# Performance work log

Hardware: AMD Instinct MI355X
Metric: run time of the kernel (lower is better)

## Reference

```python
import jax, jax.numpy as jnp
import numpy as np

B, S, HID = 4, 2048, 2048
H, HKV, D = 16, 4, 128
RANK = 512
SCALE = D ** -0.5


def setup_inputs() -> dict:
    key = jax.random.key(0)
    ks = jax.random.split(key, 5)
    scale_w = 0.02
    return {
        "hidden_states": jax.random.normal(ks[0], (B, S, HID), dtype=jnp.float32),
        "Wq": jax.random.normal(ks[1], (HID, H * D), dtype=jnp.float32) * scale_w,
        "Wc": jax.random.normal(ks[2], (HID, RANK), dtype=jnp.float32) * scale_w,
        "Wup": jax.random.normal(ks[3], (RANK, HKV * D), dtype=jnp.float32) * scale_w,
        "Wo": jax.random.normal(ks[4], (H * D, HID), dtype=jnp.float32) * scale_w,
    }


def reference(hidden_states, Wq, Wc, Wup, Wo):
    b, s, _ = hidden_states.shape
    n_rep = H // HKV
    # Q projection -> (b, H, s, D)
    q = (hidden_states @ Wq).reshape(b, s, H, D).transpose(0, 2, 1, 3)
    # low-rank KV compression -> (b, s, RANK)
    kv_c = hidden_states @ Wc
    # gate in source is ones -> sigmoid(1) constant scalar multiply
    kv_c = kv_c * jax.nn.sigmoid(jnp.float32(1.0))
    # decompress: single kv_up_proj produces shared K/V content
    kv = (kv_c @ Wup).reshape(b, s, HKV, D).transpose(0, 2, 1, 3)  # (b, HKV, s, D)
    k = jnp.repeat(kv, n_rep, axis=1)  # (b, H, s, D), repeat_interleave over heads
    v = k
    scores = jnp.einsum("bhqd,bhkd->bhqk", q, k) * SCALE
    attn = jax.nn.softmax(scores.astype(jnp.float32), axis=-1).astype(q.dtype)
    out = jnp.einsum("bhqk,bhkd->bhqd", attn, v)
    out = out.transpose(0, 2, 1, 3).reshape(b, s, H * D)
    return out @ Wo
```

## Files before the change

kernel.cpp:

```cpp
#include <hip/hip_runtime.h>
#include <hip/hip_bf16.h>
#include <stdint.h>

#define DEV __device__ __forceinline__

typedef __bf16 bf16x8 __attribute__((ext_vector_type(8)));
typedef float f32x4 __attribute__((ext_vector_type(4)));
typedef float f32x16 __attribute__((ext_vector_type(16)));
typedef int i32x4 __attribute__((ext_vector_type(4)));


DEV void gload_lds16(const void* g, void* l) {
  __builtin_amdgcn_global_load_lds((const __attribute__((address_space(1))) void*)g,
                                   (__attribute__((address_space(3))) void*)l, 16, 0, 0);
}

__global__ __launch_bounds__(256) void k_cast(const float* __restrict__ in,
                                              __hip_bfloat16* __restrict__ out, int n) {
  int i = (blockIdx.x * 256 + threadIdx.x) * 8;
  if (i >= n) return;
  const float4* p = (const float4*)(in + i);
  float4 a = p[0], c = p[1];
  bf16x8 v;
  v[0] = (__bf16)a.x; v[1] = (__bf16)a.y; v[2] = (__bf16)a.z; v[3] = (__bf16)a.w;
  v[4] = (__bf16)c.x; v[5] = (__bf16)c.y; v[6] = (__bf16)c.z; v[7] = (__bf16)c.w;
  *(bf16x8*)(out + i) = v;
}

__global__ __launch_bounds__(256) void k_tcast(const float* __restrict__ in,
                                               __hip_bfloat16* __restrict__ out, int R, int C) {
  __shared__ float t[32][33];
  int c0 = blockIdx.x * 32, r0 = blockIdx.y * 32;
  int x = threadIdx.x, y0 = threadIdx.y;
  for (int j = y0; j < 32; j += 8) t[j][x] = in[(size_t)(r0 + j) * C + c0 + x];
  __syncthreads();
  for (int j = y0; j < 32; j += 8)
    out[(size_t)(c0 + j) * R + r0 + x] = __float2bfloat16(t[x][j]);
}

__global__ __launch_bounds__(256) void k_tbf16(const __hip_bfloat16* __restrict__ in,
                                               __hip_bfloat16* __restrict__ out) {
  __shared__ unsigned short t[32][33];
  int z = blockIdx.z;
  const unsigned short* ip = (const unsigned short*)in + (size_t)z * 2048 * 128;
  unsigned short* op = (unsigned short*)out + (size_t)z * 2048 * 128;
  int d0 = blockIdx.x * 32, s0 = blockIdx.y * 32;
  int x = threadIdx.x, y0 = threadIdx.y;
  for (int j = y0; j < 32; j += 8) t[j][x] = ip[(size_t)(s0 + j) * 128 + d0 + x];
  __syncthreads();
  for (int j = y0; j < 32; j += 8) op[(size_t)(d0 + j) * 2048 + s0 + x] = t[x][j];
}

template <int MODE>
__global__ __launch_bounds__(256, 2) void k_gemm(const __hip_bfloat16* __restrict__ A,
                                                 const __hip_bfloat16* __restrict__ BT,
                                                 void* __restrict__ Cout,
                                                 int M, int N, int K, float scale) {
  __shared__ __align__(16) __hip_bfloat16 As[128 * 64];
  __shared__ __align__(16) __hip_bfloat16 Bs[128 * 64];
  const int tid = threadIdx.x;
  const int lane = tid & 63, wid = tid >> 6;
  const int g = lane >> 4, lr = lane & 15;
  const int m0 = blockIdx.x * 128, n0 = blockIdx.y * 128;
  const int wr = wid >> 1, wc = wid & 1;
  const f32x4 vzero = {0.f, 0.f, 0.f, 0.f};

  f32x4 acc[4][4];
#pragma unroll
  for (int i = 0; i < 4; ++i)
#pragma unroll
    for (int j = 0; j < 4; ++j) acc[i][j] = vzero;

  const char* aSrc[4];
  const char* bSrc[4];
  char* aDst[4];
  char* bDst[4];
#pragma unroll
  for (int i = 0; i < 4; ++i) {
    int p = i * 4096 + tid * 16;
    int row = p >> 7, colb = p & 127;
    int scol = colb ^ ((row & 7) << 4);
    aSrc[i] = (const char*)A + ((size_t)(m0 + row) * K) * 2 + scol;
    bSrc[i] = (const char*)BT + ((size_t)(n0 + row) * K) * 2 + scol;
    aDst[i] = (char*)As + i * 4096 + wid * 1024;
    bDst[i] = (char*)Bs + i * 4096 + wid * 1024;
  }

  const int nk = K >> 6;
  for (int kt = 0; kt < nk; ++kt) {
    const size_t ko = (size_t)kt * 128;
#pragma unroll
    for (int i = 0; i < 4; ++i) gload_lds16(aSrc[i] + ko, aDst[i]);
#pragma unroll
    for (int i = 0; i < 4; ++i) gload_lds16(bSrc[i] + ko, bDst[i]);
    __syncthreads();
#pragma unroll
    for (int kc = 0; kc < 2; ++kc) {
      bf16x8 af[4], bfr[4];
#pragma unroll
      for (int fm = 0; fm < 4; ++fm) {
        int row = wr * 64 + fm * 16 + lr;
        int cb = (kc * 64 + g * 16) ^ ((row & 7) << 4);
        af[fm] = *(const bf16x8*)((const char*)As + row * 128 + cb);
      }
#pragma unroll
      for (int fn = 0; fn < 4; ++fn) {
        int row = wc * 64 + fn * 16 + lr;
        int cb = (kc * 64 + g * 16) ^ ((row & 7) << 4);
        bfr[fn] = *(const bf16x8*)((const char*)Bs + row * 128 + cb);
      }
#pragma unroll
      for (int fm = 0; fm < 4; ++fm)
#pragma unroll
        for (int fn = 0; fn < 4; ++fn)
          acc[fm][fn] =
              __builtin_amdgcn_mfma_f32_16x16x32_bf16(af[fm], bfr[fn], acc[fm][fn], 0, 0, 0);
    }
    __syncthreads();
  }

#pragma unroll
  for (int fm = 0; fm < 4; ++fm) {
#pragma unroll
    for (int fn = 0; fn < 4; ++fn) {
      const int mb = m0 + wr * 64 + fm * 16 + g * 4;
      const int n = n0 + wc * 64 + fn * 16 + lr;
#pragma unroll
      for (int r = 0; r < 4; ++r) {
        float v = acc[fm][fn][r] * scale;
        int m = mb + r;
        if constexpr (MODE == 0) {
          ((float*)Cout)[(size_t)m * N + n] = v;
        } else if constexpr (MODE == 1) {
          int b = m >> 11, s = m & 2047, h = n >> 7, d = n & 127;
          ((__hip_bfloat16*)Cout)[(((size_t)(b * 16 + h) * 2048) + s) * 128 + d] =
              __float2bfloat16(v);
        } else if constexpr (MODE == 2) {
          int b = m >> 11, s = m & 2047, hk = n >> 7, d = n & 127;
          ((__hip_bfloat16*)Cout)[(((size_t)(b * 4 + hk) * 2048) + s) * 128 + d] =
              __float2bfloat16(v);
        } else {
          ((__hip_bfloat16*)Cout)[(size_t)n * M + m] = __float2bfloat16(v);
        }
      }
    }
  }
}

__global__ __launch_bounds__(512, 2) void k_attn2(const __hip_bfloat16* __restrict__ q,
                                                  const __hip_bfloat16* __restrict__ kv,
                                                  const __hip_bfloat16* __restrict__ kvT,
                                                  __hip_bfloat16* __restrict__ out) {
  __shared__ __align__(16) char smem[65536];
  const int tid = threadIdx.x, lane = tid & 63, wid = tid >> 6;
  const int hi = lane >> 5, lq = lane & 31;
  const int qt = blockIdx.x;
  const int pair = blockIdx.y;
  const int b = pair >> 2, hkv = pair & 3;
  const int h = hkv * 4 + (wid & 3);
  const int q0w = qt * 64 + (wid >> 2) * 32;

  const char* qrow =
      (const char*)q + (((size_t)(b * 16 + h) * 2048 + q0w + lq) * 128 + hi * 8) * 2;
  bf16x8 qfr[8];
#pragma unroll
  for (int kt = 0; kt < 8; ++kt) qfr[kt] = *(const bf16x8*)(qrow + kt * 32);

  const char* kbase = (const char*)kv + ((size_t)pair * 2048 * 128) * 2;
  const char* tbase = (const char*)kvT + ((size_t)pair * 2048 * 128) * 2;
  const char* pK;
  const char* pV;
  {
    int p0 = tid * 16;
    int krow = p0 >> 8, kcol = p0 & 255;
    pK = kbase + (size_t)krow * 256 + (kcol ^ ((krow & 15) << 4));
    int vrow = p0 >> 7, vcol = p0 & 127;
    pV = tbase + (size_t)vrow * 4096 + (vcol ^ ((vrow & 7) << 4));
  }

  f32x16 accO[4];
#pragma unroll
  for (int dt = 0; dt < 4; ++dt)
#pragma unroll
    for (int i = 0; i < 16; ++i) accO[dt][i] = 0.f;
  float m_run = -1e30f, l_run = 0.f;

  const int hsK = (hi * 16) ^ ((lq & 15) << 4);
  const int hsV = (hi * 16) ^ ((lq & 7) << 4);

  auto stage = [&](int kb, int vb) {
    gload_lds16(pK, smem + kb + wid * 1024);
    gload_lds16(pK + 8192, smem + kb + 8192 + wid * 1024);
    gload_lds16(pV, smem + vb + wid * 1024);
    gload_lds16(pV + 262144, smem + vb + 8192 + wid * 1024);
    pK += 16384;
    pV += 128;
  };

  auto compute = [&](int kb, int vb) {
    f32x16 st[2];
#pragma unroll
    for (int i = 0; i < 16; ++i) { st[0][i] = 0.f; st[1][i] = 0.f; }
    const char* Kb = smem + kb;
#pragma unroll
    for (int tau = 0; tau < 2; ++tau) {
      const char* Kr = Kb + (tau * 32 + lq) * 256;
#pragma unroll
      for (int kt = 0; kt < 8; ++kt) {
        bf16x8 kf = *(const bf16x8*)(Kr + ((kt * 32) ^ hsK));
        st[tau] = __builtin_amdgcn_mfma_f32_32x32x16_bf16(kf, qfr[kt], st[tau], 0, 0, 0);
      }
    }
    float mloc[8];
#pragma unroll
    for (int i = 0; i < 8; ++i)
      mloc[i] = fmaxf(fmaxf(st[0][i], st[0][i + 8]), fmaxf(st[1][i], st[1][i + 8]));
#pragma unroll
    for (int i = 0; i < 4; ++i) mloc[i] = fmaxf(mloc[i], mloc[i + 4]);
    float pm = fmaxf(fmaxf(mloc[0], mloc[1]), fmaxf(mloc[2], mloc[3]));
    pm = fmaxf(pm, __shfl_xor(pm, 32));
    if (__any(pm > m_run + 8.f)) {
      float mnew = fmaxf(m_run, pm);
      float alpha = __builtin_amdgcn_exp2f(m_run - mnew);
      m_run = mnew;
      l_run *= alpha;
#pragma unroll
      for (int dt = 0; dt < 4; ++dt)
#pragma unroll
        for (int i = 0; i < 16; ++i) accO[dt][i] *= alpha;
    }
    float p0[16], p1[16];
#pragma unroll
    for (int i = 0; i < 16; ++i) p0[i] = __builtin_amdgcn_exp2f(st[0][i] - m_run);
#pragma unroll
    for (int i = 0; i < 16; ++i) p1[i] = __builtin_amdgcn_exp2f(st[1][i] - m_run);
    float s0 = 0.f, s1 = 0.f, s2 = 0.f, s3 = 0.f;
#pragma unroll
    for (int i = 0; i < 8; ++i) {
      s0 += p0[i]; s1 += p0[i + 8]; s2 += p1[i]; s3 += p1[i + 8];
    }
    l_run += (s0 + s1) + (s2 + s3);
    bf16x8 pfr[4];
#pragma unroll
    for (int ks = 0; ks < 4; ++ks) {
      const int base = (ks & 1) * 8;
      int A0, A1, B0, B1;
      if (ks < 2) {
        asm("v_cvt_pk_bf16_f32 %0, %1, %2" : "=v"(A0) : "v"(p0[base + 0]), "v"(p0[base + 1]));
        asm("v_cvt_pk_bf16_f32 %0, %1, %2" : "=v"(A1) : "v"(p0[base + 2]), "v"(p0[base + 3]));
        asm("v_cvt_pk_bf16_f32 %0, %1, %2" : "=v"(B0) : "v"(p0[base + 4]), "v"(p0[base + 5]));
        asm("v_cvt_pk_bf16_f32 %0, %1, %2" : "=v"(B1) : "v"(p0[base + 6]), "v"(p0[base + 7]));
      } else {
        asm("v_cvt_pk_bf16_f32 %0, %1, %2" : "=v"(A0) : "v"(p1[base + 0]), "v"(p1[base + 1]));
        asm("v_cvt_pk_bf16_f32 %0, %1, %2" : "=v"(A1) : "v"(p1[base + 2]), "v"(p1[base + 3]));
        asm("v_cvt_pk_bf16_f32 %0, %1, %2" : "=v"(B0) : "v"(p1[base + 4]), "v"(p1[base + 5]));
        asm("v_cvt_pk_bf16_f32 %0, %1, %2" : "=v"(B1) : "v"(p1[base + 6]), "v"(p1[base + 7]));
      }
      asm("v_permlane32_swap_b32 %0, %1" : "+v"(A0), "+v"(B0));
      asm("v_permlane32_swap_b32 %0, %1" : "+v"(A1), "+v"(B1));
      union { int w[4]; bf16x8 v; } u;
      u.w[0] = A0; u.w[1] = A1; u.w[2] = B0; u.w[3] = B1;
      pfr[ks] = u.v;
    }
    const char* Vb = smem + vb;
#pragma unroll
    for (int dt = 0; dt < 4; ++dt) {
      const char* Vr = Vb + (dt * 32 + lq) * 128;
#pragma unroll
      for (int ks = 0; ks < 4; ++ks) {
        bf16x8 vf = *(const bf16x8*)(Vr + ((ks * 32) ^ hsV));
        accO[dt] = __builtin_amdgcn_mfma_f32_32x32x16_bf16(vf, pfr[ks], accO[dt], 0, 0, 0);
      }
    }
  };

  stage(0, 32768);
  __syncthreads();
#pragma unroll 1
  for (int it = 0; it < 16; ++it) {
    stage(16384, 49152);
    compute(0, 32768);
    __syncthreads();
    if (it < 15) stage(0, 32768);
    compute(16384, 49152);
    __syncthreads();
  }

  float lt = l_run + __shfl_xor(l_run, 32);
  float inv = 1.f / lt;
#pragma unroll
  for (int dt = 0; dt < 4; ++dt)
#pragma unroll
    for (int i = 0; i < 16; ++i) accO[dt][i] *= inv;

  __syncthreads();
  char* scr = smem + wid * 8192;
  const int swq = (lq & 15) << 4;
#pragma unroll
  for (int dt = 0; dt < 4; ++dt) {
#pragma unroll
    for (int rp = 0; rp < 8; ++rp) {
      int w;
      asm("v_cvt_pk_bf16_f32 %0, %1, %2"
          : "=v"(w)
          : "v"(accO[dt][2 * rp]), "v"(accO[dt][2 * rp + 1]));
      int dloc = ((2 * rp) & 3) + 8 * (rp >> 1) + 4 * hi;
      int bytec = (dt * 64 + dloc * 2) ^ swq;
      *(int*)(scr + lq * 256 + bytec) = w;
    }
  }
  __syncthreads();
  const int l16 = lane & 15, lh = lane >> 4;
#pragma unroll
  for (int ps = 0; ps < 8; ++ps) {
    int qr = ps * 4 + lh;
    i32x4 v = *(const i32x4*)(scr + qr * 256 + ((l16 * 16) ^ ((qr & 15) << 4)));
    char* dst = (char*)out + (((size_t)(b * 2048 + q0w + qr) * 2048) + h * 128 + l16 * 8) * 2;
    *(i32x4*)dst = v;
  }
}

extern "C" void kernel_launch(void* const* d_in, const int* in_sizes, int n_in,
                              void* d_out, int out_size, void* d_ws, size_t ws_size,
                              hipStream_t stream) {
  const float* hs = (const float*)d_in[0];
  const float* Wq = (const float*)d_in[1];
  const float* Wc = (const float*)d_in[2];
  const float* Wup = (const float*)d_in[3];
  const float* Wo = (const float*)d_in[4];

  if (ws_size < 105381888u) return;
  char* ws = (char*)d_ws;
  __hip_bfloat16* hs_bf = (__hip_bfloat16*)(ws + 0);
  __hip_bfloat16* q_attn = (__hip_bfloat16*)(ws + 33554432);
  __hip_bfloat16* kvb = (__hip_bfloat16*)(ws + 67108864);
  __hip_bfloat16* kvT = (__hip_bfloat16*)(ws + 75497472);
  __hip_bfloat16* WqT = (__hip_bfloat16*)(ws + 83886080);
  __hip_bfloat16* WoT = (__hip_bfloat16*)(ws + 92274688);
  __hip_bfloat16* WupT = (__hip_bfloat16*)(ws + 100663296);
  __hip_bfloat16* Wc_bf = (__hip_bfloat16*)(ws + 101187584);
  __hip_bfloat16* WckvT = (__hip_bfloat16*)(ws + 103284736);
  __hip_bfloat16* attnout = hs_bf;

  const float qscale = (float)(0.08838834764831845 * 1.4426950408889634);

  k_cast<<<8192, 256, 0, stream>>>(hs, hs_bf, 16777216);
  k_cast<<<512, 256, 0, stream>>>(Wc, Wc_bf, 1048576);
  k_tcast<<<dim3(64, 64), dim3(32, 8), 0, stream>>>(Wq, WqT, 2048, 2048);
  k_tcast<<<dim3(64, 64), dim3(32, 8), 0, stream>>>(Wo, WoT, 2048, 2048);
  k_tcast<<<dim3(16, 16), dim3(32, 8), 0, stream>>>(Wup, WupT, 512, 512);
  k_gemm<3><<<dim3(16, 4), 256, 0, stream>>>(Wc_bf, WupT, WckvT, 2048, 512, 512,
                                             0.7310585786300049f);
  k_gemm<1><<<dim3(64, 16), 256, 0, stream>>>(hs_bf, WqT, q_attn, 8192, 2048, 2048, qscale);
  k_gemm<2><<<dim3(64, 4), 256, 0, stream>>>(hs_bf, WckvT, kvb, 8192, 512, 2048, 1.0f);
  k_tbf16<<<dim3(4, 64, 16), dim3(32, 8), 0, stream>>>(kvb, kvT);
  k_attn2<<<dim3(32, 16), 512, 0, stream>>>(q_attn, kvb, kvT, attnout);
  k_gemm<0><<<dim3(64, 16), 256, 0, stream>>>(attnout, WoT, d_out, 8192, 2048, 2048, 1.0f);
}
```

Baseline: 355.6 us.

## Add 256x256-tile pipelined GEMM kernel for Q and output projections

Introduces a new 512-thread GEMM kernel with 256x256 output tiles, double-buffered direct global-to-LDS loads, swizzled LDS layout, explicit waitcnt/barrier scheduling and MFMA priority hints. It replaces the 128x128 kernel for the two large 8192x2048x2048 projections, raising arithmetic intensity per tile and overlapping loads with MFMAs. The tradeoffs are heavy LDS use (128KB) and high register pressure, which may limit occupancy, and only 256 blocks, which may fill the GPU poorly.

```diff
diff --git a/kernel.cpp b/kernel.cpp
--- a/kernel.cpp
+++ b/kernel.cpp
@@ -129,18 +129,146 @@
       for (int r = 0; r < 4; ++r) {
         float v = acc[fm][fn][r] * scale;
         int m = mb + r;
-        if constexpr (MODE == 0) {
-          ((float*)Cout)[(size_t)m * N + n] = v;
-        } else if constexpr (MODE == 1) {
-          int b = m >> 11, s = m & 2047, h = n >> 7, d = n & 127;
-          ((__hip_bfloat16*)Cout)[(((size_t)(b * 16 + h) * 2048) + s) * 128 + d] =
-              __float2bfloat16(v);
-        } else if constexpr (MODE == 2) {
+        if constexpr (MODE == 2) {
           int b = m >> 11, s = m & 2047, hk = n >> 7, d = n & 127;
           ((__hip_bfloat16*)Cout)[(((size_t)(b * 4 + hk) * 2048) + s) * 128 + d] =
               __float2bfloat16(v);
         } else {
           ((__hip_bfloat16*)Cout)[(size_t)n * M + m] = __float2bfloat16(v);
+        }
+      }
+    }
+  }
+}
+
+template <int MODE>
+__global__ __launch_bounds__(512, 2) void k_gemm256(const __hip_bfloat16* __restrict__ A,
+                                                    const __hip_bfloat16* __restrict__ BT,
+                                                    void* __restrict__ Cout,
+                                                    int M, int N, int K, float scale) {
+  __shared__ __align__(16) char smem[131072];
+  const int tid = threadIdx.x;
+  const int lane = tid & 63, wid = tid >> 6;
+  const int lr = lane & 15, g = lane >> 4;
+  const int m0 = blockIdx.x * 256, n0 = blockIdx.y * 256;
+  const int wr = wid >> 2, wc = wid & 3;
+  const size_t K2 = (size_t)K * 2;
+  const f32x4 vzero = {0.f, 0.f, 0.f, 0.f};
+
+  const char *sA0, *sA1, *sB0, *sB1;
+  {
+    int p = tid * 16;
+    int row = p >> 6;
+    int slot = (p >> 4) & 3;
+    int sw = (slot ^ ((row >> 1) & 3)) << 4;
+    sA0 = (const char*)A + (size_t)(m0 + row) * K2 + sw;
+    sA1 = (const char*)A + (size_t)(m0 + row + 128) * K2 + sw;
+    sB0 = (const char*)BT + (size_t)(n0 + row) * K2 + sw;
+    sB1 = (const char*)BT + (size_t)(n0 + row + 128) * K2 + sw;
+  }
+  char* const ldsW = smem + wid * 1024;
+
+  auto stA = [&](int buf, int kc, size_t koT) {
+    char* hb = ldsW + buf * 65536 + kc * 16384;
+    gload_lds16(sA0 + koT + (kc << 6), hb);
+    gload_lds16(sA1 + koT + (kc << 6), hb + 8192);
+  };
+  auto stB = [&](int buf, int kc, size_t koT) {
+    char* hb = ldsW + buf * 65536 + 32768 + kc * 16384;
+    gload_lds16(sB0 + koT + (kc << 6), hb);
+    gload_lds16(sB1 + koT + (kc << 6), hb + 8192);
+  };
+
+  const int swr = ((g ^ ((lr >> 1) & 3)) << 4);
+  const char* rdA = smem + wr * 8192 + lr * 64 + swr;
+  const char* rdB = smem + 32768 + wc * 4096 + lr * 64 + swr;
+
+  f32x4 acc[8][4];
+#pragma unroll
+  for (int i = 0; i < 8; ++i)
+#pragma unroll
+    for (int j = 0; j < 4; ++j) acc[i][j] = vzero;
+
+  stA(0, 0, 0); stB(0, 0, 0); stA(0, 1, 0); stB(0, 1, 0);
+
+  auto mfma16 = [&](bf16x8* af, bf16x8* bfv, int mh) {
+    __builtin_amdgcn_s_setprio(1);
+#pragma unroll
+    for (int f = 0; f < 4; ++f)
+#pragma unroll
+      for (int n = 0; n < 4; ++n)
+        acc[mh * 4 + f][n] =
+            __builtin_amdgcn_mfma_f32_16x16x32_bf16(af[f], bfv[n], acc[mh * 4 + f][n], 0, 0, 0);
+    __builtin_amdgcn_s_setprio(0);
+  };
+
+  auto tileK = [&](int buf, size_t koNext, bool doStage, bool last) {
+    asm volatile("s_waitcnt vmcnt(4)" ::: "memory");
+    __builtin_amdgcn_s_barrier();
+    bf16x8 a[4], b[4];
+    if (doStage) stA(buf ^ 1, 0, koNext);
+#pragma unroll
+    for (int n = 0; n < 4; ++n) b[n] = *(const bf16x8*)(rdB + buf * 65536 + n * 1024);
+#pragma unroll
+    for (int f = 0; f < 4; ++f) a[f] = *(const bf16x8*)(rdA + buf * 65536 + f * 1024);
+    asm volatile("s_waitcnt lgkmcnt(0)" ::: "memory");
+    __builtin_amdgcn_sched_barrier(0);
+    mfma16(a, b, 0);
+    if (doStage) stB(buf ^ 1, 0, koNext);
+#pragma unroll
+    for (int f = 0; f < 4; ++f) a[f] = *(const bf16x8*)(rdA + buf * 65536 + 4096 + f * 1024);
+    asm volatile("s_waitcnt lgkmcnt(0)" ::: "memory");
+    __builtin_amdgcn_sched_barrier(0);
+    mfma16(a, b, 1);
+    if (last) {
+      asm volatile("s_waitcnt vmcnt(0)" ::: "memory");
+    } else {
+      asm volatile("s_waitcnt vmcnt(4)" ::: "memory");
+    }
+    __builtin_amdgcn_s_barrier();
+    if (doStage) stA(buf ^ 1, 1, koNext);
+#pragma unroll
+    for (int n = 0; n < 4; ++n) b[n] = *(const bf16x8*)(rdB + buf * 65536 + 16384 + n * 1024);
+#pragma unroll
+    for (int f = 0; f < 4; ++f) a[f] = *(const bf16x8*)(rdA + buf * 65536 + 16384 + f * 1024);
+    asm volatile("s_waitcnt lgkmcnt(0)" ::: "memory");
+    __builtin_amdgcn_sched_barrier(0);
+    mfma16(a, b, 0);
+    if (doStage) stB(buf ^ 1, 1, koNext);
+#pragma unroll
+    for (int f = 0; f < 4; ++f)
+      a[f] = *(const bf16x8*)(rdA + buf * 65536 + 16384 + 4096 + f * 1024);
+    asm volatile("s_waitcnt lgkmcnt(0)" ::: "memory");
+    __builtin_amdgcn_sched_barrier(0);
+    mfma16(a, b, 1);
+  };
+
+  const int nk = K >> 6;
+  size_t ko = 128;
+#pragma unroll 1
+  for (int it = 0; it < (nk - 2) / 2; ++it) {
+    tileK(0, ko, true, false); ko += 128;
+    tileK(1, ko, true, false); ko += 128;
+  }
+  tileK(0, ko, true, false);
+  tileK(1, 0, false, true);
+
+#pragma unroll
+  for (int fm = 0; fm < 8; ++fm) {
+#pragma unroll
+    for (int fn = 0; fn < 4; ++fn) {
+      const int mb = m0 + wr * 128 + fm * 16 + g * 4;
+      const int n = n0 + wc * 64 + fn * 16 + lr;
+#pragma unroll
+      for (int r = 0; r < 4; ++r) {
+        float v = acc[fm][fn][r] * scale;
+        int m = mb + r;
+        if constexpr (MODE == 0) {
+          ((float*)Cout)[(size_t)m * N + n] = v;
+        } else {
+          int b = m >> 11, s = m & 2047, h = n >> 7, d = n & 127;
+          ((__hip_bfloat16*)Cout)[(((size_t)(b * 16 + h) * 2048) + s) * 128 + d] =
+              __float2bfloat16(v);
         }
       }
     }
@@ -351,9 +479,9 @@
   k_tcast<<<dim3(16, 16), dim3(32, 8), 0, stream>>>(Wup, WupT, 512, 512);
   k_gemm<3><<<dim3(16, 4), 256, 0, stream>>>(Wc_bf, WupT, WckvT, 2048, 512, 512,
                                              0.7310585786300049f);
-  k_gemm<1><<<dim3(64, 16), 256, 0, stream>>>(hs_bf, WqT, q_attn, 8192, 2048, 2048, qscale);
+  k_gemm256<1><<<dim3(32, 8), 512, 0, stream>>>(hs_bf, WqT, q_attn, 8192, 2048, 2048, qscale);
   k_gemm<2><<<dim3(64, 4), 256, 0, stream>>>(hs_bf, WckvT, kvb, 8192, 512, 2048, 1.0f);
   k_tbf16<<<dim3(4, 64, 16), dim3(32, 8), 0, stream>>>(kvb, kvT);
   k_attn2<<<dim3(32, 16), 512, 0, stream>>>(q_attn, kvb, kvT, attnout);
-  k_gemm<0><<<dim3(64, 16), 256, 0, stream>>>(attnout, WoT, d_out, 8192, 2048, 2048, 1.0f);
-}
+  k_gemm256<0><<<dim3(32, 8), 512, 0, stream>>>(attnout, WoT, d_out, 8192, 2048, 2048, 1.0f);
+}
```

Measured after the change: 350.8 us. Within noise of the previous version (-1.4%).
